# Optimization experiments

Hardware: AMD Instinct MI355X
Metric: run time of the kernel (lower is better)

The kernel has to match this reference:

```python
import jax, jax.numpy as jnp
import numpy as np

N = 50000
E = 1600000
IN_C = 128
HID = 128
OUT_C = 64


def setup_inputs() -> dict:
    key = jax.random.key(0)
    ks = jax.random.split(key, 10)
    x = jax.random.normal(ks[0], (N, IN_C), dtype=jnp.float32)
    edge_index = jax.random.randint(ks[1], (2, E), 0, N, dtype=jnp.int64)
    s = lambda fan_in: 1.0 / np.sqrt(fan_in)
    W1 = jax.random.uniform(ks[2], (HID, IN_C), jnp.float32, -s(IN_C), s(IN_C))
    b1 = jnp.zeros((HID,), jnp.float32)
    Wc = jax.random.uniform(ks[3], (HID, HID + IN_C), jnp.float32, -s(HID + IN_C), s(HID + IN_C))
    bc = jax.random.uniform(ks[4], (HID,), jnp.float32, -s(HID + IN_C), s(HID + IN_C))
    W2 = jax.random.uniform(ks[5], (HID, HID), jnp.float32, -s(HID), s(HID))
    b2 = jnp.zeros((HID,), jnp.float32)
    Wo = jax.random.uniform(ks[6], (OUT_C, 2 * HID), jnp.float32, -s(2 * HID), s(2 * HID))
    bo = jax.random.uniform(ks[7], (OUT_C,), jnp.float32, -s(2 * HID), s(2 * HID))
    return {"x": x, "edge_index": edge_index, "W1": W1, "b1": b1,
            "Wc": Wc, "bc": bc, "W2": W2, "b2": b2, "Wo": Wo, "bo": bo}


def _gcn_conv(x, src, dst, norm, W, b):
    # PyG GCNConv: h = x @ W^T, propagate with sym-norm coeffs, add bias.
    h = x @ W.T                                   # [N, F_out]
    msg = h[src] * norm[:, None]                  # gather + scale, [E+N, F_out]
    out = jax.ops.segment_sum(msg, dst, num_segments=N)  # scatter-add
    return out + b


def _norm_coeffs(edge_index):
    # add self-loops, then sym normalization: D^{-1/2} A_hat D^{-1/2}
    loop = jnp.arange(N, dtype=edge_index.dtype)
    src = jnp.concatenate([edge_index[0], loop])
    dst = jnp.concatenate([edge_index[1], loop])
    deg = jax.ops.segment_sum(jnp.ones_like(dst, dtype=jnp.float32), dst, num_segments=N)
    dis = jnp.where(deg > 0, jax.lax.rsqrt(deg), 0.0)
    norm = dis[src] * dis[dst]
    return src, dst, norm


def reference(x, edge_index, W1, b1, Wc, bc, W2, b2, Wo, bo):
    src, dst, norm = _norm_coeffs(edge_index)
    x_agg = jax.nn.relu(_gcn_conv(x, src, dst, norm, W1, b1))
    x_comb = jnp.concatenate([x_agg, x], axis=1)
    x_comb = jax.nn.relu(x_comb @ Wc.T + bc)
    # dropout is identity in eval mode
    x_agg2 = _gcn_conv(x_comb, src, dst, norm, W2, b2)
    x_out = jnp.concatenate([x_agg2, x_comb], axis=1)
    return x_out @ Wo.T + bo
```

## Files before the change

kernel.cpp:

```cpp
#include <hip/hip_runtime.h>
#include <hip/hip_fp16.h>

#define Nn 50000
#define Ee 1600000
#define NRANGE 196
#define CAP 10240
#define CHUNK 4096

typedef __attribute__((ext_vector_type(8))) short short8;
typedef __attribute__((ext_vector_type(4))) float f32x4;
typedef unsigned short ushort;
typedef unsigned int uint;

__device__ __forceinline__ ushort f32_to_bf16(float f) {
    unsigned u = __builtin_bit_cast(unsigned, f);
    unsigned r = u + 0x7FFFu + ((u >> 16) & 1u);
    return (ushort)(r >> 16);
}
__device__ __forceinline__ float bf16_to_f32(ushort h) {
    unsigned u = ((unsigned)h) << 16;
    return __builtin_bit_cast(float, u);
}


__global__ __launch_bounds__(256) void partition_kernel(const int* __restrict__ ei,
                                                        int* __restrict__ gcursor,
                                                        int2* __restrict__ buckets) {
    __shared__ int cnt[NRANGE];
    __shared__ int cur[NRANGE];
    int t = threadIdx.x;
    if (t < NRANGE) cnt[t] = 0;
    __syncthreads();
    int base = blockIdx.x * CHUNK;
    const int* __restrict__ dst = ei + Ee;
    #pragma unroll
    for (int k = 0; k < CHUNK / 256; ++k) {
        int e = base + k * 256 + t;
        if (e < Ee) atomicAdd(&cnt[dst[e] >> 8], 1);
    }
    __syncthreads();
    if (t < NRANGE) cur[t] = atomicAdd(&gcursor[t], cnt[t]);
    __syncthreads();
    #pragma unroll
    for (int k = 0; k < CHUNK / 256; ++k) {
        int e = base + k * 256 + t;
        if (e < Ee) {
            int d = dst[e];
            int r = d >> 8;
            int slot = atomicAdd(&cur[r], 1);
            if (slot < CAP) buckets[r * CAP + slot] = make_int2(ei[e], d);
        }
    }
}

__global__ __launch_bounds__(256) void count_kernel(const int2* __restrict__ buckets,
                                                    const int* __restrict__ gcursor,
                                                    int* __restrict__ counts,
                                                    float* __restrict__ dis) {
    __shared__ int cnt[256];
    int r = blockIdx.x, t = threadIdx.x;
    cnt[t] = 0;
    __syncthreads();
    int n = gcursor[r]; n = (n < CAP) ? n : CAP;
    const int2* b = buckets + (size_t)r * CAP;
    for (int i = t; i < n; i += 256) {
        int2 p = b[i];
        atomicAdd(&cnt[p.y & 255], 1);
    }
    __syncthreads();
    int node = r * 256 + t;
    if (node < Nn) {
        counts[node] = cnt[t];
        dis[node] = rsqrtf((float)(cnt[t] + 1));
    }
}

__global__ void scan1_kernel(const int* __restrict__ counts, int* __restrict__ offsets,
                             int* __restrict__ partials) {
    __shared__ int sd[256];
    int t = threadIdx.x;
    int i = blockIdx.x * 256 + t;
    int cp = 0;
    if (i < Nn) cp = (counts[i] + 7) & ~7;
    int v = cp;
    #pragma unroll
    for (int off = 1; off < 256; off <<= 1) {
        sd[t] = v; __syncthreads();
        int add = (t >= off) ? sd[t - off] : 0;
        __syncthreads();
        v += add;
    }
    if (i < Nn) offsets[i] = v - cp;
    if (t == 255) partials[blockIdx.x] = v;
}

__global__ void scan3_kernel(int* __restrict__ offsets, const int* __restrict__ partials,
                             const int* __restrict__ counts, int* __restrict__ csr) {
    __shared__ int sd[256];
    int t = threadIdx.x;
    int s = (t < blockIdx.x) ? partials[t] : 0;
    sd[t] = s; __syncthreads();
    #pragma unroll
    for (int off = 128; off > 0; off >>= 1) {
        if (t < off) sd[t] += sd[t + off];
        __syncthreads();
    }
    int base = sd[0];
    int i = blockIdx.x * 256 + t;
    if (i < Nn) {
        int off = offsets[i] + base;
        offsets[i] = off;
        int deg = counts[i];
        int cp  = (deg + 7) & ~7;
        for (int j = off + deg; j < off + cp; ++j) csr[j] = Nn;
        if (i == Nn - 1) offsets[Nn] = off + cp;
    }
}

__global__ __launch_bounds__(256) void fill_kernel(const int2* __restrict__ buckets,
                                                   const int* __restrict__ gcursor,
                                                   const int* __restrict__ offsets,
                                                   int* __restrict__ csr) {
    __shared__ int cur[256];
    int r = blockIdx.x, t = threadIdx.x;
    int node = r * 256 + t;
    cur[t] = (node < Nn) ? offsets[node] : 0;
    __syncthreads();
    int n = gcursor[r]; n = (n < CAP) ? n : CAP;
    const int2* b = buckets + (size_t)r * CAP;
    for (int i = t; i < n; i += 256) {
        int2 p = b[i];
        int pos = atomicAdd(&cur[p.y & 255], 1);
        csr[pos] = p.x;
    }
}

__global__ void prep_w_kernel(const float* __restrict__ W1, const float* __restrict__ Wc,
                              const float* __restrict__ W2, const float* __restrict__ Wo,
                              ushort* __restrict__ base) {
    int i = blockIdx.x * 256 + threadIdx.x;
    const float* src; ushort* hi; ushort* lo; int idx;
    if (i < 16384)      { src = W1; hi = base;          lo = base + 16384;  idx = i; }
    else if (i < 49152) { src = Wc; hi = base + 32768;  lo = base + 65536;  idx = i - 16384; }
    else if (i < 65536) { src = W2; hi = base + 98304;  lo = base + 114688; idx = i - 49152; }
    else                { src = Wo; hi = base + 131072; lo = base + 147456; idx = i - 65536; }
    float f = src[idx];
    ushort hb = f32_to_bf16(f);
    hi[idx] = hb;
    lo[idx] = f32_to_bf16(f - bf16_to_f32(hb));
}

__global__ void split_x_kernel(const float* __restrict__ x, ushort* __restrict__ xhi,
                               ushort* __restrict__ xlo) {
    int i = (blockIdx.x * 256 + threadIdx.x) * 4;
    float4 v = *(const float4*)(x + i);
    float vv[4] = {v.x, v.y, v.z, v.w};
    ushort h[4], l[4];
    #pragma unroll
    for (int j = 0; j < 4; ++j) {
        h[j] = f32_to_bf16(vv[j]);
        l[j] = f32_to_bf16(vv[j] - bf16_to_f32(h[j]));
    }
    *(uint2*)(xhi + i) = make_uint2((uint)h[0] | ((uint)h[1] << 16),
                                    (uint)h[2] | ((uint)h[3] << 16));
    *(uint2*)(xlo + i) = make_uint2((uint)l[0] | ((uint)l[1] << 16),
                                    (uint)l[2] | ((uint)l[3] << 16));
}

template <int CO, int K, bool RELU, bool HASBIAS, bool SCALEDIS, int OUTMODE>
__global__ __launch_bounds__(256, 3) void mfma_gemm(
    const ushort* __restrict__ AH0, const ushort* __restrict__ AL0,
    const ushort* __restrict__ AH1, const ushort* __restrict__ AL1,
    const ushort* __restrict__ Whi, const ushort* __restrict__ Wlo,
    const float* __restrict__ bias, const float* __restrict__ dis,
    void* __restrict__ outp, ushort* __restrict__ outLo) {
    constexpr int NF = CO / 16;
    constexpr int NCH = K / 64;
    constexpr int WISS = CO / 32;

    __shared__ ushort lds[2 * 64 * 64 + 2 * CO * 64];
    ushort* ldsAh = lds;
    ushort* ldsAl = lds + 64 * 64;
    ushort* ldsWh = lds + 2 * 64 * 64;
    ushort* ldsWl = ldsWh + CO * 64;

    int tid  = threadIdx.x;
    int wave = tid >> 6;
    int lane = tid & 63;
    int c = lane & 15;
    int g = lane >> 4;
    int row0 = blockIdx.x * 64;

    f32x4 acc1[NF], acc2[NF];
    #pragma unroll
    for (int f = 0; f < NF; ++f) {
        acc1[f] = (f32x4){0.f, 0.f, 0.f, 0.f};
        acc2[f] = (f32x4){0.f, 0.f, 0.f, 0.f};
    }

    #pragma unroll
    for (int ch = 0; ch < NCH; ++ch) {
        const int k0 = ch * 64;
        const ushort* Ah = (K == 256 && k0 >= 128) ? AH1 : AH0;
        const ushort* Al = (K == 256 && k0 >= 128) ? AL1 : AL0;
        const int kb = (K == 256 && k0 >= 128) ? (k0 - 128) : k0;

        #pragma unroll
        for (int i = 0; i < 2; ++i) {
            int idx = tid + i * 256;
            int row = idx >> 3, kg = idx & 7;
            int gr = row0 + row; gr = (gr < Nn) ? gr : (Nn - 1);
            int sb = (kg * 16) ^ ((row & 7) << 4);
            int ldsoff = (i * 256 + wave * 64) * 8;
            __builtin_amdgcn_global_load_lds(Ah + (size_t)gr * 128 + kb + (sb >> 1),
                                             &ldsAh[ldsoff], 16, 0, 0);
            __builtin_amdgcn_global_load_lds(Al + (size_t)gr * 128 + kb + (sb >> 1),
                                             &ldsAl[ldsoff], 16, 0, 0);
        }
        #pragma unroll
        for (int i = 0; i < WISS; ++i) {
            int idx = tid + i * 256;
            int col = idx >> 3, kg = idx & 7;
            int sb = (kg * 16) ^ ((col & 7) << 4);
            int ldsoff = (i * 256 + wave * 64) * 8;
            __builtin_amdgcn_global_load_lds(Whi + (size_t)col * K + k0 + (sb >> 1),
                                             &ldsWh[ldsoff], 16, 0, 0);
            __builtin_amdgcn_global_load_lds(Wlo + (size_t)col * K + k0 + (sb >> 1),
                                             &ldsWl[ldsoff], 16, 0, 0);
        }
        __syncthreads();

        #pragma unroll
        for (int s = 0; s < 2; ++s) {
            int arow = wave * 16 + c;
            int ab = (s * 64 + g * 16) ^ ((arow & 7) << 4);
            short8 ahi = *(const short8*)((const char*)ldsAh + arow * 128 + ab);
            short8 alo = *(const short8*)((const char*)ldsAl + arow * 128 + ab);
            #pragma unroll
            for (int f = 0; f < NF; ++f) {
                int col = f * 16 + c;
                int wb = (s * 64 + g * 16) ^ ((col & 7) << 4);
                short8 bh = *(const short8*)((const char*)ldsWh + col * 128 + wb);
                short8 bl = *(const short8*)((const char*)ldsWl + col * 128 + wb);
                acc1[f] = __builtin_amdgcn_mfma_f32_16x16x32_bf16(ahi, bh, acc1[f], 0, 0, 0);
                acc2[f] = __builtin_amdgcn_mfma_f32_16x16x32_bf16(ahi, bl, acc2[f], 0, 0, 0);
                acc2[f] = __builtin_amdgcn_mfma_f32_16x16x32_bf16(alo, bh, acc2[f], 0, 0, 0);
            }
        }
        __syncthreads();
    }

    #pragma unroll
    for (int f = 0; f < NF; ++f) {
        int col = f * 16 + c;
        float bv = HASBIAS ? bias[col] : 0.f;
        #pragma unroll
        for (int rg = 0; rg < 4; ++rg) {
            int row = row0 + wave * 16 + g * 4 + rg;
            if (row < Nn) {
                float v = acc1[f][rg] + acc2[f][rg] + bv;
                if (RELU) v = fmaxf(v, 0.f);
                if (SCALEDIS) v *= dis[row];
                size_t idx = (size_t)row * CO + col;
                if constexpr (OUTMODE == 1) {
                    ((__half*)outp)[idx] = __float2half_rn(v);
                } else if constexpr (OUTMODE == 2) {
                    ushort hb = f32_to_bf16(v);
                    ((ushort*)outp)[idx] = hb;
                    outLo[idx] = f32_to_bf16(v - bf16_to_f32(hb));
                } else {
                    ((float*)outp)[idx] = v;
                }
            }
        }
    }
}

template <bool RELU>
__global__ __launch_bounds__(256) void propagate_kernel(
    const __half* __restrict__ gbuf, const int* __restrict__ offs,
    const int* __restrict__ csr, const float* __restrict__ dis,
    const float* __restrict__ bias, ushort* __restrict__ outHi,
    ushort* __restrict__ outLo) {
    int node = blockIdx.x * 4 + (threadIdx.x >> 6);
    if (node >= Nn) return;
    int lane = threadIdx.x & 63;
    float2 sv = __half22float2(*((const __half2*)(gbuf + ((size_t)node << 7)) + lane));
    float ax = sv.x, ay = sv.y;
    int beg = offs[node], end = offs[node + 1];
    for (int e = beg; e < end; e += 8) {
        int s0 = csr[e],     s1 = csr[e + 1], s2 = csr[e + 2], s3 = csr[e + 3];
        int s4 = csr[e + 4], s5 = csr[e + 5], s6 = csr[e + 6], s7 = csr[e + 7];
        __half2 h0 = *((const __half2*)(gbuf + ((size_t)s0 << 7)) + lane);
        __half2 h1 = *((const __half2*)(gbuf + ((size_t)s1 << 7)) + lane);
        __half2 h2 = *((const __half2*)(gbuf + ((size_t)s2 << 7)) + lane);
        __half2 h3 = *((const __half2*)(gbuf + ((size_t)s3 << 7)) + lane);
        __half2 h4 = *((const __half2*)(gbuf + ((size_t)s4 << 7)) + lane);
        __half2 h5 = *((const __half2*)(gbuf + ((size_t)s5 << 7)) + lane);
        __half2 h6 = *((const __half2*)(gbuf + ((size_t)s6 << 7)) + lane);
        __half2 h7 = *((const __half2*)(gbuf + ((size_t)s7 << 7)) + lane);
        float2 v0 = __half22float2(h0), v1 = __half22float2(h1);
        float2 v2 = __half22float2(h2), v3 = __half22float2(h3);
        float2 v4 = __half22float2(h4), v5 = __half22float2(h5);
        float2 v6 = __half22float2(h6), v7 = __half22float2(h7);
        ax += ((v0.x + v1.x) + (v2.x + v3.x)) + ((v4.x + v5.x) + (v6.x + v7.x));
        ay += ((v0.y + v1.y) + (v2.y + v3.y)) + ((v4.y + v5.y) + (v6.y + v7.y));
    }
    float di = dis[node];
    ax = fmaf(di, ax, bias[lane * 2]);
    ay = fmaf(di, ay, bias[lane * 2 + 1]);
    if (RELU) { ax = fmaxf(ax, 0.f); ay = fmaxf(ay, 0.f); }
    ushort hx = f32_to_bf16(ax), hy = f32_to_bf16(ay);
    ushort lx = f32_to_bf16(ax - bf16_to_f32(hx));
    ushort ly = f32_to_bf16(ay - bf16_to_f32(hy));
    ((uint*)(outHi + ((size_t)node << 7)))[lane] = (uint)hx | ((uint)hy << 16);
    ((uint*)(outLo + ((size_t)node << 7)))[lane] = (uint)lx | ((uint)ly << 16);
}


extern "C" void kernel_launch(void* const* d_in, const int* in_sizes, int n_in,
                              void* d_out, int out_size, void* d_ws, size_t ws_size,
                              hipStream_t stream) {
    const float* x  = (const float*)d_in[0];
    const int*   ei = (const int*)d_in[1];
    const float* W1 = (const float*)d_in[2];
    const float* b1 = (const float*)d_in[3];
    const float* Wc = (const float*)d_in[4];
    const float* bc = (const float*)d_in[5];
    const float* W2 = (const float*)d_in[6];
    const float* b2 = (const float*)d_in[7];
    const float* Wo = (const float*)d_in[8];
    const float* bo = (const float*)d_in[9];
    float* out = (float*)d_out;

    char* base = (char*)d_ws;
    auto carve = [&](size_t bytes) {
        void* p = (void*)base;
        base += (bytes + 255) & ~(size_t)255;
        return p;
    };
    char*  tmp      = (char*)carve(512 * 1024);
    int*   gcursor  = (int*)tmp;
    int*   counts   = (int*)(tmp + 1024);
    ushort* wplanes = (ushort*)tmp;
    int*   offsets  = (int*)carve((Nn + 1) * sizeof(int));
    int*   partials = (int*)carve(256 * sizeof(int));
    float* dis      = (float*)carve(Nn * sizeof(float));
    int2*  buckets  = (int2*)carve((size_t)NRANGE * CAP * sizeof(int2));
    int*   csr      = (int*)carve(((size_t)Ee + 8 * Nn) * sizeof(int));
    __half* gbuf    = (__half*)carve((size_t)(Nn + 2) * 128 * sizeof(__half));
    ushort* xhi     = (ushort*)carve((size_t)Nn * 128 * sizeof(ushort));
    ushort* xlo     = (ushort*)carve((size_t)Nn * 128 * sizeof(ushort));
    ushort* aggHi   = (ushort*)carve((size_t)Nn * 128 * sizeof(ushort));
    ushort* aggLo   = (ushort*)carve((size_t)Nn * 128 * sizeof(ushort));
    ushort* combHi  = (ushort*)carve((size_t)Nn * 128 * sizeof(ushort));
    ushort* combLo  = (ushort*)carve((size_t)Nn * 128 * sizeof(ushort));

    const ushort* w1hi = wplanes;
    const ushort* w1lo = wplanes + 16384;
    const ushort* wchi = wplanes + 32768;
    const ushort* wclo = wplanes + 65536;
    const ushort* w2hi = wplanes + 98304;
    const ushort* w2lo = wplanes + 114688;
    const ushort* wohi = wplanes + 131072;
    const ushort* wolo = wplanes + 147456;

    const int SCAN_BLOCKS = (Nn + 255) / 256;
    const int PBLOCKS = (Ee + CHUNK - 1) / CHUNK;

    hipMemsetAsync(gcursor, 0, NRANGE * sizeof(int), stream);
    hipMemsetAsync(gbuf + (size_t)Nn * 128, 0, 256, stream);
    partition_kernel<<<PBLOCKS, 256, 0, stream>>>(ei, gcursor, buckets);
    count_kernel<<<NRANGE, 256, 0, stream>>>(buckets, gcursor, counts, dis);
    scan1_kernel<<<SCAN_BLOCKS, 256, 0, stream>>>(counts, offsets, partials);
    scan3_kernel<<<SCAN_BLOCKS, 256, 0, stream>>>(offsets, partials, counts, csr);
    fill_kernel<<<NRANGE, 256, 0, stream>>>(buckets, gcursor, offsets, csr);

    prep_w_kernel<<<320, 256, 0, stream>>>(W1, Wc, W2, Wo, (ushort*)wplanes);
    split_x_kernel<<<6250, 256, 0, stream>>>(x, xhi, xlo);

    const int GB = (Nn + 63) / 64;
    const int PB = (Nn + 3) / 4;

    mfma_gemm<128, 128, false, false, true, 1><<<GB, 256, 0, stream>>>(
        xhi, xlo, nullptr, nullptr, w1hi, w1lo, nullptr, dis, gbuf, nullptr);
    propagate_kernel<true><<<PB, 256, 0, stream>>>(gbuf, offsets, csr, dis, b1, aggHi, aggLo);
    mfma_gemm<128, 256, true, true, false, 2><<<GB, 256, 0, stream>>>(
        aggHi, aggLo, xhi, xlo, wchi, wclo, bc, nullptr, combHi, combLo);
    mfma_gemm<128, 128, false, false, true, 1><<<GB, 256, 0, stream>>>(
        combHi, combLo, nullptr, nullptr, w2hi, w2lo, nullptr, dis, gbuf, nullptr);
    propagate_kernel<false><<<PB, 256, 0, stream>>>(gbuf, offsets, csr, dis, b2, aggHi, aggLo);
    mfma_gemm<64, 256, false, true, false, 0><<<GB, 256, 0, stream>>>(
        aggHi, aggLo, combHi, combLo, wohi, wolo, bo, nullptr, out, nullptr);
}
```

Measured before the change: 339.9 us.

## Pack bucket entries into 32 bits, merge prep kernels, sum gathered rows in half2

Bucket entries shrink from an int2 pair to one packed uint (source << 8 | low byte of destination), which halves the bucket write and read traffic in partition, count and fill. The weight-split and x-split kernels merge into one launch to save a kernel launch. The propagate inner loop sums the eight gathered fp16 neighbour rows with half2 adds before converting to float, cutting conversions but lowering accumulation precision to fp16 for each group of eight.

```diff
diff --git a/kernel.cpp b/kernel.cpp
--- a/kernel.cpp
+++ b/kernel.cpp
@@ -25,7 +25,7 @@
 
 __global__ __launch_bounds__(256) void partition_kernel(const int* __restrict__ ei,
                                                         int* __restrict__ gcursor,
-                                                        int2* __restrict__ buckets) {
+                                                        uint* __restrict__ buckets) {
     __shared__ int cnt[NRANGE];
     __shared__ int cur[NRANGE];
     int t = threadIdx.x;
@@ -48,12 +48,12 @@
             int d = dst[e];
             int r = d >> 8;
             int slot = atomicAdd(&cur[r], 1);
-            if (slot < CAP) buckets[r * CAP + slot] = make_int2(ei[e], d);
-        }
-    }
-}
-
-__global__ __launch_bounds__(256) void count_kernel(const int2* __restrict__ buckets,
+            if (slot < CAP) buckets[r * CAP + slot] = ((uint)ei[e] << 8) | (uint)(d & 255);
+        }
+    }
+}
+
+__global__ __launch_bounds__(256) void count_kernel(const uint* __restrict__ buckets,
                                                     const int* __restrict__ gcursor,
                                                     int* __restrict__ counts,
                                                     float* __restrict__ dis) {
@@ -62,10 +62,9 @@
     cnt[t] = 0;
     __syncthreads();
     int n = gcursor[r]; n = (n < CAP) ? n : CAP;
-    const int2* b = buckets + (size_t)r * CAP;
+    const uint* b = buckets + (size_t)r * CAP;
     for (int i = t; i < n; i += 256) {
-        int2 p = b[i];
-        atomicAdd(&cnt[p.y & 255], 1);
+        atomicAdd(&cnt[b[i] & 255u], 1);
     }
     __syncthreads();
     int node = r * 256 + t;
@@ -117,7 +116,7 @@
     }
 }
 
-__global__ __launch_bounds__(256) void fill_kernel(const int2* __restrict__ buckets,
+__global__ __launch_bounds__(256) void fill_kernel(const uint* __restrict__ buckets,
                                                    const int* __restrict__ gcursor,
                                                    const int* __restrict__ offsets,
                                                    int* __restrict__ csr) {
@@ -127,44 +126,45 @@
     cur[t] = (node < Nn) ? offsets[node] : 0;
     __syncthreads();
     int n = gcursor[r]; n = (n < CAP) ? n : CAP;
-    const int2* b = buckets + (size_t)r * CAP;
+    const uint* b = buckets + (size_t)r * CAP;
     for (int i = t; i < n; i += 256) {
-        int2 p = b[i];
-        int pos = atomicAdd(&cur[p.y & 255], 1);
-        csr[pos] = p.x;
-    }
-}
-
-__global__ void prep_w_kernel(const float* __restrict__ W1, const float* __restrict__ Wc,
-                              const float* __restrict__ W2, const float* __restrict__ Wo,
-                              ushort* __restrict__ base) {
-    int i = blockIdx.x * 256 + threadIdx.x;
-    const float* src; ushort* hi; ushort* lo; int idx;
-    if (i < 16384)      { src = W1; hi = base;          lo = base + 16384;  idx = i; }
-    else if (i < 49152) { src = Wc; hi = base + 32768;  lo = base + 65536;  idx = i - 16384; }
-    else if (i < 65536) { src = W2; hi = base + 98304;  lo = base + 114688; idx = i - 49152; }
-    else                { src = Wo; hi = base + 131072; lo = base + 147456; idx = i - 65536; }
-    float f = src[idx];
-    ushort hb = f32_to_bf16(f);
-    hi[idx] = hb;
-    lo[idx] = f32_to_bf16(f - bf16_to_f32(hb));
-}
-
-__global__ void split_x_kernel(const float* __restrict__ x, ushort* __restrict__ xhi,
-                               ushort* __restrict__ xlo) {
-    int i = (blockIdx.x * 256 + threadIdx.x) * 4;
-    float4 v = *(const float4*)(x + i);
-    float vv[4] = {v.x, v.y, v.z, v.w};
-    ushort h[4], l[4];
-    #pragma unroll
-    for (int j = 0; j < 4; ++j) {
-        h[j] = f32_to_bf16(vv[j]);
-        l[j] = f32_to_bf16(vv[j] - bf16_to_f32(h[j]));
-    }
-    *(uint2*)(xhi + i) = make_uint2((uint)h[0] | ((uint)h[1] << 16),
-                                    (uint)h[2] | ((uint)h[3] << 16));
-    *(uint2*)(xlo + i) = make_uint2((uint)l[0] | ((uint)l[1] << 16),
-                                    (uint)l[2] | ((uint)l[3] << 16));
+        uint p = b[i];
+        int pos = atomicAdd(&cur[p & 255u], 1);
+        csr[pos] = (int)(p >> 8);
+    }
+}
+
+__global__ void prep_split_kernel(const float* __restrict__ x, ushort* __restrict__ xhi,
+                                  ushort* __restrict__ xlo,
+                                  const float* __restrict__ W1, const float* __restrict__ Wc,
+                                  const float* __restrict__ W2, const float* __restrict__ Wo,
+                                  ushort* __restrict__ wbase) {
+    if (blockIdx.x < 6250) {
+        int i = (blockIdx.x * 256 + threadIdx.x) * 4;
+        float4 v = *(const float4*)(x + i);
+        float vv[4] = {v.x, v.y, v.z, v.w};
+        ushort h[4], l[4];
+        #pragma unroll
+        for (int j = 0; j < 4; ++j) {
+            h[j] = f32_to_bf16(vv[j]);
+            l[j] = f32_to_bf16(vv[j] - bf16_to_f32(h[j]));
+        }
+        *(uint2*)(xhi + i) = make_uint2((uint)h[0] | ((uint)h[1] << 16),
+                                        (uint)h[2] | ((uint)h[3] << 16));
+        *(uint2*)(xlo + i) = make_uint2((uint)l[0] | ((uint)l[1] << 16),
+                                        (uint)l[2] | ((uint)l[3] << 16));
+    } else {
+        int i = (blockIdx.x - 6250) * 256 + threadIdx.x;
+        const float* src; ushort* hi; ushort* lo; int idx;
+        if (i < 16384)      { src = W1; hi = wbase;          lo = wbase + 16384;  idx = i; }
+        else if (i < 49152) { src = Wc; hi = wbase + 32768;  lo = wbase + 65536;  idx = i - 16384; }
+        else if (i < 65536) { src = W2; hi = wbase + 98304;  lo = wbase + 114688; idx = i - 49152; }
+        else                { src = Wo; hi = wbase + 131072; lo = wbase + 147456; idx = i - 65536; }
+        float f = src[idx];
+        ushort hb = f32_to_bf16(f);
+        hi[idx] = hb;
+        lo[idx] = f32_to_bf16(f - bf16_to_f32(hb));
+    }
 }
 
 template <int CO, int K, bool RELU, bool HASBIAS, bool SCALEDIS, int OUTMODE>
@@ -299,12 +299,14 @@
         __half2 h5 = *((const __half2*)(gbuf + ((size_t)s5 << 7)) + lane);
         __half2 h6 = *((const __half2*)(gbuf + ((size_t)s6 << 7)) + lane);
         __half2 h7 = *((const __half2*)(gbuf + ((size_t)s7 << 7)) + lane);
-        float2 v0 = __half22float2(h0), v1 = __half22float2(h1);
-        float2 v2 = __half22float2(h2), v3 = __half22float2(h3);
-        float2 v4 = __half22float2(h4), v5 = __half22float2(h5);
-        float2 v6 = __half22float2(h6), v7 = __half22float2(h7);
-        ax += ((v0.x + v1.x) + (v2.x + v3.x)) + ((v4.x + v5.x) + (v6.x + v7.x));
-        ay += ((v0.y + v1.y) + (v2.y + v3.y)) + ((v4.y + v5.y) + (v6.y + v7.y));
+        __half2 t0 = __hadd2(h0, h1), t1 = __hadd2(h2, h3);
+        __half2 t2 = __hadd2(h4, h5), t3 = __hadd2(h6, h7);
+        t0 = __hadd2(t0, t1);
+        t2 = __hadd2(t2, t3);
+        t0 = __hadd2(t0, t2);
+        float2 v = __half22float2(t0);
+        ax += v.x;
+        ay += v.y;
     }
     float di = dis[node];
     ax = fmaf(di, ax, bias[lane * 2]);
@@ -346,7 +348,7 @@
     int*   offsets  = (int*)carve((Nn + 1) * sizeof(int));
     int*   partials = (int*)carve(256 * sizeof(int));
     float* dis      = (float*)carve(Nn * sizeof(float));
-    int2*  buckets  = (int2*)carve((size_t)NRANGE * CAP * sizeof(int2));
+    uint*  buckets  = (uint*)carve((size_t)NRANGE * CAP * sizeof(uint));
     int*   csr      = (int*)carve(((size_t)Ee + 8 * Nn) * sizeof(int));
     __half* gbuf    = (__half*)carve((size_t)(Nn + 2) * 128 * sizeof(__half));
     ushort* xhi     = (ushort*)carve((size_t)Nn * 128 * sizeof(ushort));
@@ -376,8 +378,8 @@
     scan3_kernel<<<SCAN_BLOCKS, 256, 0, stream>>>(offsets, partials, counts, csr);
     fill_kernel<<<NRANGE, 256, 0, stream>>>(buckets, gcursor, offsets, csr);
 
-    prep_w_kernel<<<320, 256, 0, stream>>>(W1, Wc, W2, Wo, (ushort*)wplanes);
-    split_x_kernel<<<6250, 256, 0, stream>>>(x, xhi, xlo);
+    prep_split_kernel<<<6570, 256, 0, stream>>>(x, xhi, xlo, W1, Wc, W2, Wo,
+                                                (ushort*)wplanes);
 
     const int GB = (Nn + 63) / 64;
     const int PB = (Nn + 3) / 4;
```

After: 331.2 us. -2.6%, faster.
